# Kernel optimization log

Measured on AMD Instinct MI355X. Metric: run time of the kernel, lower is better.

The kernel has to match this reference:

```python
import jax, jax.numpy as jnp
import numpy as np
import math

B, S, E = 4, 2048, 1024


def setup_inputs() -> dict:
    key = jax.random.key(0)
    ks = jax.random.split(key, 9)
    x = jax.random.normal(ks[0], (B, S, E), dtype=jnp.float32)
    # causal boolean mask, broadcast over batch: True = keep
    mask = jnp.broadcast_to(jnp.tril(jnp.ones((S, S), dtype=bool)), (B, S, S))
    sc = 1.0 / math.sqrt(E)
    Wq = jax.random.normal(ks[1], (E, E), dtype=jnp.float32) * sc
    bq = jnp.zeros((E,), dtype=jnp.float32)
    Wk = jax.random.normal(ks[2], (E, E), dtype=jnp.float32) * sc
    bk = jnp.zeros((E,), dtype=jnp.float32)
    Wv = jax.random.normal(ks[3], (E, E), dtype=jnp.float32) * sc
    bv = jnp.zeros((E,), dtype=jnp.float32)
    gamma = jnp.ones((E,), dtype=jnp.float32)
    beta = jnp.zeros((E,), dtype=jnp.float32)
    return {"x": x, "mask": mask, "Wq": Wq, "bq": bq, "Wk": Wk, "bk": bk,
            "Wv": Wv, "bv": bv, "gamma": gamma, "beta": beta}


def reference(x, mask, Wq, bq, Wk, bk, Wv, bv, gamma, beta):
    E_ = x.shape[-1]
    q = jnp.einsum('bse,fe->bsf', x, Wq) + bq
    k = jnp.einsum('bse,fe->bsf', x, Wk) + bk
    v = jnp.einsum('bse,fe->bsf', x, Wv) + bv
    scores = jnp.einsum('bqe,bke->bqk', q, k) / jnp.sqrt(jnp.float32(E_))
    scores = jnp.where(mask, scores, -jnp.inf)
    probs = jax.nn.softmax(scores, axis=-1)
    attn = jnp.einsum('bqk,bke->bqe', probs, v)
    y = attn + x
    # LayerNorm over last dim, eps matches torch default 1e-5
    mu = jnp.mean(y, axis=-1, keepdims=True)
    var = jnp.mean(jnp.square(y - mu), axis=-1, keepdims=True)
    return (y - mu) / jnp.sqrt(var + 1e-5) * gamma + beta
```

## Files before the change

kernel.cpp:

```cpp
#include <hip/hip_runtime.h>
#include <hip/hip_bf16.h>
#include <stdint.h>

#define B_ 4
#define S_ 2048
#define E_ 1024
#define BS_ (B_*S_)

using bf16x8 = __attribute__((ext_vector_type(8))) __bf16;
using f32x4  = __attribute__((ext_vector_type(4))) float;

__constant__ int pv_mt[24] = {7,8,9,10,11,12,13,14,15,15,14,6,13,5,12,4,11,3,10,2,9,1,8,0};
__constant__ int pv_ck[24] = {0,0,0,0,0,0,0,0,0, 1, 1,0, 1,0, 1,0, 1,0, 1,0, 1,0, 1,0};

__device__ __forceinline__ unsigned short f2bf(float f) {
  unsigned int u = __float_as_uint(f);
  u += 0x7fffu + ((u >> 16) & 1u);
  return (unsigned short)(u >> 16);
}
__device__ __forceinline__ float bf2f(unsigned short h) {
  return __uint_as_float(((unsigned int)h) << 16);
}

__device__ __forceinline__ void gld16(const unsigned short* g, unsigned short* l) {
  __builtin_amdgcn_global_load_lds((__attribute__((address_space(1))) void*)(void*)g,
                                   (__attribute__((address_space(3))) void*)l, 16, 0, 0);
}

__global__ __launch_bounds__(256) void prep_all(
    const float* __restrict__ x,
    const float* __restrict__ Wq, const float* __restrict__ Wk, const float* __restrict__ Wv,
    const float* __restrict__ bq, const float* __restrict__ bk, const float* __restrict__ bv,
    unsigned short* __restrict__ xb, unsigned short* __restrict__ Wb, float* __restrict__ bb,
    float* __restrict__ lz) {
  const int i = blockIdx.x * 256 + threadIdx.x;
  const int nx4 = BS_ * E_ / 4, nw4 = E_ * E_ / 4;
  if (i < nx4) {
    const float4 v = ((const float4*)x)[i];
    ushort4 o;
    o.x = f2bf(v.x); o.y = f2bf(v.y); o.z = f2bf(v.z); o.w = f2bf(v.w);
    ((ushort4*)xb)[i] = o;
  } else if (i < nx4 + 3 * nw4) {
    const int j = i - nx4;
    const int m = j / nw4, jj = j - m * nw4;
    const float* src = (m == 0) ? Wq : (m == 1) ? Wk : Wv;
    const float4 v = ((const float4*)src)[jj];
    ushort4 o;
    o.x = f2bf(v.x); o.y = f2bf(v.y); o.z = f2bf(v.z); o.w = f2bf(v.w);
    ((ushort4*)Wb)[j] = o;
  } else {
    const int j = i - nx4 - 3 * nw4;
    if (j < 3 * E_) bb[j] = (j < E_) ? bq[j] : (j < 2 * E_) ? bk[j - E_] : bv[j - 2 * E_];
    else { const int k = j - 3 * E_; if (k < BS_) lz[k] = 0.f; }
  }
}

template<int EPI>
__device__ __forceinline__ void gemm_body(
    const unsigned short* __restrict__ A, const unsigned short* __restrict__ Bm,
    float* __restrict__ Cf,
    unsigned short* __restrict__ Cb, unsigned short* __restrict__ VtOut,
    const float* __restrict__ bias,
    int K, int lda, int ldb, int ldc,
    long sA, long sB, long sC, float scale)
{
  constexpr int BM = 128, BN = 128, BK = 64;
  __shared__ __align__(16) unsigned short As[BM * BK];
  __shared__ __align__(16) unsigned short Bs[BN * BK];

  int mt, nt, ck = 0, bz;
  if (EPI == 1) {
    const int sig = (blockIdx.x & 7) * 68 + (blockIdx.x >> 3);
    bz = sig / 136;
    const int rem = sig - bz * 136;
    const int M = (rem >= 78) ? 3 : (rem >= 36) ? 2 : (rem >= 10) ? 1 : 0;
    const int cumM = (M == 3) ? 78 : (M == 2) ? 36 : (M == 1) ? 10 : 0;
    const int inner = rem - cumM;
    if (inner < 16 * M) {
      const int N = inner >> 4, t2 = inner & 15;
      mt = 4 * M + (t2 >> 2); nt = 4 * N + (t2 & 3);
    } else {
      const int t2 = inner - 16 * M;
      const int ml = (t2 >= 6) ? 3 : (t2 >= 3) ? 2 : (t2 >= 1) ? 1 : 0;
      const int nl = t2 - (ml * (ml + 1)) / 2;
      mt = 4 * M + ml; nt = 4 * M + nl;
    }
  } else if (EPI == 2) {
    mt = pv_mt[blockIdx.y]; ck = pv_ck[blockIdx.y]; nt = blockIdx.x; bz = blockIdx.z;
  } else {
    mt = blockIdx.y; nt = blockIdx.x; bz = blockIdx.z;
  }
  A  += sA * bz;
  Bm += sB * bz;
  const int m0 = mt * BM, n0 = nt * BN;
  const int k0s  = (EPI == 2 && ck) ? 1024 : 0;
  const int kend = (EPI == 2) ? (ck ? m0 + BM : min(1024, m0 + BM)) : K;

  const int t = threadIdx.x;
  const int lane = t & 63, wave = t >> 6;
  const int wr = wave >> 1, wc = wave & 1;
  const int q = lane >> 4, r = lane & 15;

  const int srow   = lane >> 3;
  const int schunk = (lane & 7) ^ srow;
  const long ga0 = (long)(m0 + wave * 32 + srow) * lda + schunk * 8;
  const long gb0 = (long)(n0 + wave * 32 + srow) * ldb + schunk * 8;

  f32x4 acc[4][4] = {};

  for (int k0 = k0s; k0 < kend; k0 += BK) {
#pragma unroll
    for (int s = 0; s < 4; ++s) {
      gld16(A  + ga0 + (long)s * 8 * lda + k0, &As[(wave * 32 + s * 8) * 64]);
      gld16(Bm + gb0 + (long)s * 8 * ldb + k0, &Bs[(wave * 32 + s * 8) * 64]);
    }
    __syncthreads();
#pragma unroll
    for (int kk = 0; kk < BK; kk += 32) {
      bf16x8 af[4], bfr[4];
      const int cq = (kk >> 3) + q;
#pragma unroll
      for (int i = 0; i < 4; ++i) {
        const int row = wr * 64 + i * 16 + r;
        af[i] = *(const bf16x8*)&As[(row * 8 + (cq ^ (r & 7))) * 8];
      }
#pragma unroll
      for (int j = 0; j < 4; ++j) {
        const int row = wc * 64 + j * 16 + r;
        bfr[j] = *(const bf16x8*)&Bs[(row * 8 + (cq ^ (r & 7))) * 8];
      }
#pragma unroll
      for (int i = 0; i < 4; ++i)
#pragma unroll
        for (int j = 0; j < 4; ++j)
          acc[i][j] = __builtin_amdgcn_mfma_f32_16x16x32_bf16(af[i], bfr[j], acc[i][j], 0, 0, 0);
    }
    __syncthreads();
  }

  if (EPI == 0) {
    if (n0 < 2 * E_) {
#pragma unroll
    for (int i = 0; i < 4; ++i)
#pragma unroll
      for (int j = 0; j < 4; ++j) {
        const int col = n0 + wc * 64 + j * 16 + r;
        const float bia = bias[col];
#pragma unroll
        for (int e = 0; e < 4; ++e) {
          const int rowg = m0 + wr * 64 + i * 16 + q * 4 + e;
          Cb[(long)rowg * ldc + col] = f2bf(acc[i][j][e] + bia);
        }
      }
    } else {
      unsigned short* scr = As + wave * 2048;
      const int bb = m0 >> 11;
      const int sbase = (m0 & (S_ - 1)) + wr * 64;
#pragma unroll
      for (int j = 0; j < 4; ++j) {
        const int e_base = n0 - 2 * E_ + wc * 64 + j * 16;
        const float bj = bias[n0 + wc * 64 + j * 16 + r];
#pragma unroll
        for (int i = 0; i < 4; ++i) {
          const int c = 2 * i + (q >> 1);
          const int slot = c ^ (r & 7);
          ushort4 o;
          o.x = f2bf(acc[i][j][0] + bj);
          o.y = f2bf(acc[i][j][1] + bj);
          o.z = f2bf(acc[i][j][2] + bj);
          o.w = f2bf(acc[i][j][3] + bj);
          *(ushort4*)&scr[r * 72 + slot * 8 + (q & 1) * 4] = o;
        }
#pragma unroll
        for (int it = 0; it < 2; ++it) {
          const int er = it * 8 + (lane >> 3);
          const int w = lane & 7;
          const bf16x8 vv = *(const bf16x8*)&scr[er * 72 + w * 8];
          const int so = (w ^ (er & 7)) * 8;
          *(bf16x8*)&VtOut[((long)bb * E_ + e_base + er) * S_ + sbase + so] = vv;
        }
      }
    }
  } else if (EPI == 1) {
    Cb += sC * bz;
    float* lv = Cf + (long)bz * S_;
#pragma unroll
    for (int i = 0; i < 4; ++i) {
      float rs[4] = {0.f, 0.f, 0.f, 0.f};
#pragma unroll
      for (int j = 0; j < 4; ++j) {
        const int col = n0 + wc * 64 + j * 16 + r;
#pragma unroll
        for (int e = 0; e < 4; ++e) {
          const int rowg = m0 + wr * 64 + i * 16 + q * 4 + e;
          float p = 0.f;
          if (col <= rowg) p = __expf(fminf(acc[i][j][e] * scale, 60.f));
          Cb[(long)rowg * ldc + col] = f2bf(p);
          rs[e] += p;
        }
      }
#pragma unroll
      for (int e = 0; e < 4; ++e) {
        float s = rs[e];
        s += __shfl_xor(s, 1); s += __shfl_xor(s, 2);
        s += __shfl_xor(s, 4); s += __shfl_xor(s, 8);
        if (r == 0) atomicAdd(&lv[m0 + wr * 64 + i * 16 + q * 4 + e], s);
      }
    }
  } else {
    const float* lv = Cf + (long)bz * S_;
    unsigned short* dst = (ck ? VtOut : Cb) + sC * bz;
#pragma unroll
    for (int i = 0; i < 4; ++i) {
      const int rb = m0 + wr * 64 + i * 16 + q * 4;
      const float4 l4 = *(const float4*)&lv[rb];
      const float r0 = 1.f / l4.x, r1 = 1.f / l4.y, r2 = 1.f / l4.z, r3 = 1.f / l4.w;
#pragma unroll
      for (int j = 0; j < 4; ++j) {
        const int col = n0 + wc * 64 + j * 16 + r;
        dst[(long)(rb + 0) * ldc + col] = f2bf(acc[i][j][0] * r0);
        dst[(long)(rb + 1) * ldc + col] = f2bf(acc[i][j][1] * r1);
        dst[(long)(rb + 2) * ldc + col] = f2bf(acc[i][j][2] * r2);
        dst[(long)(rb + 3) * ldc + col] = f2bf(acc[i][j][3] * r3);
      }
    }
  }
}

__global__ __launch_bounds__(256, 4) void gemm_qkv(
    const unsigned short* A, const unsigned short* Bm, float* Cf,
    unsigned short* Cb, unsigned short* VtOut, const float* bias,
    int K, int lda, int ldb, int ldc, long sA, long sB, long sC, float scale) {
  gemm_body<0>(A, Bm, Cf, Cb, VtOut, bias, K, lda, ldb, ldc, sA, sB, sC, scale);
}
__global__ __launch_bounds__(256, 4) void gemm_sc(
    const unsigned short* A, const unsigned short* Bm, float* Cf,
    unsigned short* Cb, unsigned short* VtOut, const float* bias,
    int K, int lda, int ldb, int ldc, long sA, long sB, long sC, float scale) {
  gemm_body<1>(A, Bm, Cf, Cb, VtOut, bias, K, lda, ldb, ldc, sA, sB, sC, scale);
}
__global__ __launch_bounds__(256, 4) void gemm_pv(
    const unsigned short* A, const unsigned short* Bm, float* Cf,
    unsigned short* Cb, unsigned short* VtOut, const float* bias,
    int K, int lda, int ldb, int ldc, long sA, long sB, long sC, float scale) {
  gemm_body<2>(A, Bm, Cf, Cb, VtOut, bias, K, lda, ldb, ldc, sA, sB, sC, scale);
}

__global__ __launch_bounds__(256) void residual_ln(
    const unsigned short* __restrict__ attn, const unsigned short* __restrict__ attn2,
    const unsigned short* __restrict__ xb,
    const float* __restrict__ gamma, const float* __restrict__ beta,
    float* __restrict__ out) {
  __shared__ float rs[4], rs2[4];
  const long row = blockIdx.x;
  const int t = threadIdx.x;
  const int lane = t & 63, wave = t >> 6;
  const ushort4 a  = ((const ushort4*)(attn + row * E_))[t];
  const ushort4 xv = ((const ushort4*)(xb + row * E_))[t];
  ushort4 b2 = make_ushort4(0, 0, 0, 0);
  if ((row & (S_ - 1)) >= 1024) b2 = ((const ushort4*)(attn2 + row * E_))[t];
  const float y0 = bf2f(a.x) + bf2f(b2.x) + bf2f(xv.x);
  const float y1 = bf2f(a.y) + bf2f(b2.y) + bf2f(xv.y);
  const float y2 = bf2f(a.z) + bf2f(b2.z) + bf2f(xv.z);
  const float y3 = bf2f(a.w) + bf2f(b2.w) + bf2f(xv.w);
  float s  = y0 + y1 + y2 + y3;
  float s2 = y0 * y0 + y1 * y1 + y2 * y2 + y3 * y3;
#pragma unroll
  for (int o = 32; o; o >>= 1) { s += __shfl_xor(s, o); s2 += __shfl_xor(s2, o); }
  if (lane == 0) { rs[wave] = s; rs2[wave] = s2; }
  __syncthreads();
  s  = rs[0] + rs[1] + rs[2] + rs[3];
  s2 = rs2[0] + rs2[1] + rs2[2] + rs2[3];
  const float mu  = s * (1.0f / E_);
  const float var = s2 * (1.0f / E_) - mu * mu;
  const float inv = rsqrtf(var + 1e-5f);
  const float4 g  = ((const float4*)gamma)[t];
  const float4 be = ((const float4*)beta)[t];
  float4 o;
  o.x = (y0 - mu) * inv * g.x + be.x;
  o.y = (y1 - mu) * inv * g.y + be.y;
  o.z = (y2 - mu) * inv * g.z + be.z;
  o.w = (y3 - mu) * inv * g.w + be.w;
  ((float4*)(out + row * E_))[t] = o;
}

extern "C" void kernel_launch(void* const* d_in, const int* in_sizes, int n_in,
                              void* d_out, int out_size, void* d_ws, size_t ws_size,
                              hipStream_t stream) {
  const float* x  = (const float*)d_in[0];
  const float* Wq = (const float*)d_in[2];
  const float* bq = (const float*)d_in[3];
  const float* Wk = (const float*)d_in[4];
  const float* bk = (const float*)d_in[5];
  const float* Wv = (const float*)d_in[6];
  const float* bv = (const float*)d_in[7];
  const float* gamma = (const float*)d_in[8];
  const float* beta  = (const float*)d_in[9];
  float* out = (float*)d_out;

  char* ws = (char*)d_ws;
  size_t off = 0;
  auto alloc = [&](size_t bytes) { char* p = ws + off; off += (bytes + 255) & ~(size_t)255; return p; };
  unsigned short* xb    = (unsigned short*)alloc((size_t)BS_ * E_ * 2);
  unsigned short* Wqkvb = (unsigned short*)alloc((size_t)3 * E_ * E_ * 2);
  float*          bqkv  = (float*)alloc((size_t)3 * E_ * 4);
  unsigned short* Cqkv  = (unsigned short*)alloc((size_t)BS_ * 2 * E_ * 2);
  unsigned short* Vt    = (unsigned short*)alloc((size_t)BS_ * E_ * 2);
  unsigned short* Sc    = (unsigned short*)alloc((size_t)B_ * S_ * S_ * 2);
  float*          lrow  = (float*)alloc((size_t)BS_ * 4);
  unsigned short* attn  = (unsigned short*)Cqkv;
  unsigned short* attn2 = (unsigned short*)Cqkv + (size_t)BS_ * E_;

  const int nprep = BS_ * E_ / 4 + 3 * E_ * E_ / 4 + 3 * E_ + BS_;
  prep_all<<<dim3((nprep + 255) / 256), 256, 0, stream>>>(x, Wq, Wk, Wv, bq, bk, bv,
                                                          xb, Wqkvb, bqkv, lrow);

  dim3 g1(3 * E_ / 128, BS_ / 128, 1);
  gemm_qkv<<<g1, 256, 0, stream>>>(xb, Wqkvb, nullptr, Cqkv, Vt, bqkv,
                                   E_, E_, E_, 2 * E_, 0, 0, 0, 1.f);

  gemm_sc<<<dim3(544), 256, 0, stream>>>(Cqkv, Cqkv + E_, lrow, Sc, nullptr, nullptr,
                                         E_, 2 * E_, 2 * E_, S_,
                                         (long)S_ * 2 * E_, (long)S_ * 2 * E_, (long)S_ * S_,
                                         0.03125f);

  dim3 g3(E_ / 128, 24, B_);
  gemm_pv<<<g3, 256, 0, stream>>>(Sc, Vt, lrow, attn, attn2, nullptr,
                                  S_, S_, S_, E_,
                                  (long)S_ * S_, (long)S_ * E_, (long)S_ * E_, 1.f);

  residual_ln<<<dim3(BS_), 256, 0, stream>>>(attn, attn2, xb, gamma, beta, out);
}
```

Measured before the change: 268.5 us.

## Use 256x256 tiles with 8 waves and a 4-stage LDS pipeline

Rewrites the shared GEMM body to use 256x256 output tiles with 512 threads. K-slices of 32 are cycled through a 4-deep LDS ring buffer, with prefetch three tiles ahead and waits on vmcnt counts in place of the load/sync/compute loop. The causal-tile schedules for scores and PV are recomputed for the larger tiles. The V-transpose epilogue now writes directly instead of going through an LDS scratch. Larger tiles cut global traffic per FLOP but produce fewer blocks (144 for scores), and they waste more compute on masked diagonal tiles.

Result: slower. 335.0 us (+24.8%).

```diff
diff --git a/kernel.cpp b/kernel.cpp
--- a/kernel.cpp
+++ b/kernel.cpp
@@ -10,8 +10,8 @@
 using bf16x8 = __attribute__((ext_vector_type(8))) __bf16;
 using f32x4  = __attribute__((ext_vector_type(4))) float;
 
-__constant__ int pv_mt[24] = {7,8,9,10,11,12,13,14,15,15,14,6,13,5,12,4,11,3,10,2,9,1,8,0};
-__constant__ int pv_ck[24] = {0,0,0,0,0,0,0,0,0, 1, 1,0, 1,0, 1,0, 1,0, 1,0, 1,0, 1,0};
+__constant__ int pv_mt2[12] = {3,4,5,6,7,7,2,6,1,5,0,4};
+__constant__ int pv_ck2[12] = {0,0,0,0,0,1,0,1,0,1,0,1};
 
 __device__ __forceinline__ unsigned short f2bf(float f) {
   unsigned int u = __float_as_uint(f);
@@ -64,29 +64,19 @@
     int K, int lda, int ldb, int ldc,
     long sA, long sB, long sC, float scale)
 {
-  constexpr int BM = 128, BN = 128, BK = 64;
-  __shared__ __align__(16) unsigned short As[BM * BK];
-  __shared__ __align__(16) unsigned short Bs[BN * BK];
+  constexpr int BM = 256, BN = 256, BK = 32;
+  __shared__ __align__(16) unsigned short As[4][BM * BK];
+  __shared__ __align__(16) unsigned short Bs[4][BN * BK];
 
   int mt, nt, ck = 0, bz;
   if (EPI == 1) {
-    const int sig = (blockIdx.x & 7) * 68 + (blockIdx.x >> 3);
-    bz = sig / 136;
-    const int rem = sig - bz * 136;
-    const int M = (rem >= 78) ? 3 : (rem >= 36) ? 2 : (rem >= 10) ? 1 : 0;
-    const int cumM = (M == 3) ? 78 : (M == 2) ? 36 : (M == 1) ? 10 : 0;
-    const int inner = rem - cumM;
-    if (inner < 16 * M) {
-      const int N = inner >> 4, t2 = inner & 15;
-      mt = 4 * M + (t2 >> 2); nt = 4 * N + (t2 & 3);
-    } else {
-      const int t2 = inner - 16 * M;
-      const int ml = (t2 >= 6) ? 3 : (t2 >= 3) ? 2 : (t2 >= 1) ? 1 : 0;
-      const int nl = t2 - (ml * (ml + 1)) / 2;
-      mt = 4 * M + ml; nt = 4 * M + nl;
-    }
+    bz = blockIdx.x / 36;
+    int rem = blockIdx.x - bz * 36;
+    int m = 0, base2 = 0;
+    while (base2 + m + 1 <= rem) { base2 += m + 1; ++m; }
+    mt = m; nt = rem - base2;
   } else if (EPI == 2) {
-    mt = pv_mt[blockIdx.y]; ck = pv_ck[blockIdx.y]; nt = blockIdx.x; bz = blockIdx.z;
+    mt = pv_mt2[blockIdx.y]; ck = pv_ck2[blockIdx.y]; nt = blockIdx.x; bz = blockIdx.z;
   } else {
     mt = blockIdx.y; nt = blockIdx.x; bz = blockIdx.z;
   }
@@ -95,107 +85,109 @@
   const int m0 = mt * BM, n0 = nt * BN;
   const int k0s  = (EPI == 2 && ck) ? 1024 : 0;
   const int kend = (EPI == 2) ? (ck ? m0 + BM : min(1024, m0 + BM)) : K;
+  const int nT = (kend - k0s) >> 5;
 
   const int t = threadIdx.x;
   const int lane = t & 63, wave = t >> 6;
-  const int wr = wave >> 1, wc = wave & 1;
+  const int wr = wave >> 2, wc = wave & 3;
   const int q = lane >> 4, r = lane & 15;
 
-  const int srow   = lane >> 3;
-  const int schunk = (lane & 7) ^ srow;
-  const long ga0 = (long)(m0 + wave * 32 + srow) * lda + schunk * 8;
-  const long gb0 = (long)(n0 + wave * 32 + srow) * ldb + schunk * 8;
-
-  f32x4 acc[4][4] = {};
-
-  for (int k0 = k0s; k0 < kend; k0 += BK) {
-#pragma unroll
-    for (int s = 0; s < 4; ++s) {
-      gld16(A  + ga0 + (long)s * 8 * lda + k0, &As[(wave * 32 + s * 8) * 64]);
-      gld16(Bm + gb0 + (long)s * 8 * ldb + k0, &Bs[(wave * 32 + s * 8) * 64]);
-    }
-    __syncthreads();
-#pragma unroll
-    for (int kk = 0; kk < BK; kk += 32) {
-      bf16x8 af[4], bfr[4];
-      const int cq = (kk >> 3) + q;
-#pragma unroll
-      for (int i = 0; i < 4; ++i) {
-        const int row = wr * 64 + i * 16 + r;
-        af[i] = *(const bf16x8*)&As[(row * 8 + (cq ^ (r & 7))) * 8];
-      }
-#pragma unroll
-      for (int j = 0; j < 4; ++j) {
-        const int row = wc * 64 + j * 16 + r;
-        bfr[j] = *(const bf16x8*)&Bs[(row * 8 + (cq ^ (r & 7))) * 8];
-      }
-#pragma unroll
-      for (int i = 0; i < 4; ++i)
-#pragma unroll
-        for (int j = 0; j < 4; ++j)
-          acc[i][j] = __builtin_amdgcn_mfma_f32_16x16x32_bf16(af[i], bfr[j], acc[i][j], 0, 0, 0);
-    }
-    __syncthreads();
+  const int srow   = lane >> 2;
+  const int schunk = (lane & 3) ^ ((lane >> 3) & 3);
+  const long ga0 = (long)(m0 + wave * 32 + srow) * lda + schunk * 8 + k0s;
+  const long gb0 = (long)(n0 + wave * 32 + srow) * ldb + schunk * 8 + k0s;
+
+  auto STAGE = [&](int tile) {
+    const int buf = tile & 3;
+    const long ko = (long)tile << 5;
+    gld16(A  + ga0 + ko,            &As[buf][wave * 1024]);
+    gld16(A  + ga0 + 16 * lda + ko, &As[buf][wave * 1024 + 512]);
+    gld16(Bm + gb0 + ko,            &Bs[buf][wave * 1024]);
+    gld16(Bm + gb0 + 16 * ldb + ko, &Bs[buf][wave * 1024 + 512]);
+  };
+
+  f32x4 acc[8][4] = {};
+
+  STAGE(0); STAGE(1); STAGE(2);
+
+  const int ca    = (q ^ ((r >> 1) & 3)) * 8;
+  const int arow0 = wr * 128 + r;
+  const int brow0 = wc * 64 + r;
+
+  for (int tt = 0; tt < nT; ++tt) {
+    if (nT - tt > 2)       asm volatile("s_waitcnt vmcnt(8)" ::: "memory");
+    else if (nT - tt == 2) asm volatile("s_waitcnt vmcnt(4)" ::: "memory");
+    else                   asm volatile("s_waitcnt vmcnt(0)" ::: "memory");
+    __builtin_amdgcn_s_barrier();
+    asm volatile("" ::: "memory");
+    if (tt + 3 < nT) STAGE(tt + 3);
+
+    const unsigned short* as_ = As[tt & 3];
+    const unsigned short* bs_ = Bs[tt & 3];
+    bf16x8 af[8], bfv[4];
+#pragma unroll
+    for (int i = 0; i < 8; ++i)
+      af[i] = *(const bf16x8*)&as_[(arow0 + i * 16) * 32 + ca];
+#pragma unroll
+    for (int j = 0; j < 4; ++j)
+      bfv[j] = *(const bf16x8*)&bs_[(brow0 + j * 16) * 32 + ca];
+
+    __builtin_amdgcn_s_setprio(1);
+#pragma unroll
+    for (int i = 0; i < 8; ++i)
+#pragma unroll
+      for (int j = 0; j < 4; ++j)
+        acc[i][j] = __builtin_amdgcn_mfma_f32_16x16x32_bf16(af[i], bfv[j], acc[i][j], 0, 0, 0);
+    __builtin_amdgcn_s_setprio(0);
   }
 
   if (EPI == 0) {
     if (n0 < 2 * E_) {
 #pragma unroll
-    for (int i = 0; i < 4; ++i)
+      for (int i = 0; i < 8; ++i)
+#pragma unroll
+        for (int j = 0; j < 4; ++j) {
+          const int col = n0 + wc * 64 + j * 16 + r;
+          const float bia = bias[col];
+          const int rowg = m0 + wr * 128 + i * 16 + q * 4;
+#pragma unroll
+          for (int e = 0; e < 4; ++e)
+            Cb[(long)(rowg + e) * ldc + col] = f2bf(acc[i][j][e] + bia);
+        }
+    } else {
+      const int bb = m0 >> 11;
+      const int sb = (m0 & (S_ - 1)) + wr * 128;
 #pragma unroll
       for (int j = 0; j < 4; ++j) {
         const int col = n0 + wc * 64 + j * 16 + r;
         const float bia = bias[col];
-#pragma unroll
-        for (int e = 0; e < 4; ++e) {
-          const int rowg = m0 + wr * 64 + i * 16 + q * 4 + e;
-          Cb[(long)rowg * ldc + col] = f2bf(acc[i][j][e] + bia);
-        }
-      }
-    } else {
-      unsigned short* scr = As + wave * 2048;
-      const int bb = m0 >> 11;
-      const int sbase = (m0 & (S_ - 1)) + wr * 64;
-#pragma unroll
-      for (int j = 0; j < 4; ++j) {
-        const int e_base = n0 - 2 * E_ + wc * 64 + j * 16;
-        const float bj = bias[n0 + wc * 64 + j * 16 + r];
-#pragma unroll
-        for (int i = 0; i < 4; ++i) {
-          const int c = 2 * i + (q >> 1);
-          const int slot = c ^ (r & 7);
+        const long ebase = (long)bb * E_ + (col - 2 * E_);
+#pragma unroll
+        for (int i = 0; i < 8; ++i) {
           ushort4 o;
-          o.x = f2bf(acc[i][j][0] + bj);
-          o.y = f2bf(acc[i][j][1] + bj);
-          o.z = f2bf(acc[i][j][2] + bj);
-          o.w = f2bf(acc[i][j][3] + bj);
-          *(ushort4*)&scr[r * 72 + slot * 8 + (q & 1) * 4] = o;
-        }
-#pragma unroll
-        for (int it = 0; it < 2; ++it) {
-          const int er = it * 8 + (lane >> 3);
-          const int w = lane & 7;
-          const bf16x8 vv = *(const bf16x8*)&scr[er * 72 + w * 8];
-          const int so = (w ^ (er & 7)) * 8;
-          *(bf16x8*)&VtOut[((long)bb * E_ + e_base + er) * S_ + sbase + so] = vv;
+          o.x = f2bf(acc[i][j][0] + bia);
+          o.y = f2bf(acc[i][j][1] + bia);
+          o.z = f2bf(acc[i][j][2] + bia);
+          o.w = f2bf(acc[i][j][3] + bia);
+          *(ushort4*)&VtOut[ebase * S_ + sb + i * 16 + q * 4] = o;
         }
       }
     }
   } else if (EPI == 1) {
-    Cb += sC * bz;
+    unsigned short* Cbz = Cb + sC * bz;
     float* lv = Cf + (long)bz * S_;
 #pragma unroll
-    for (int i = 0; i < 4; ++i) {
+    for (int i = 0; i < 8; ++i) {
       float rs[4] = {0.f, 0.f, 0.f, 0.f};
+      const int rowg0 = m0 + wr * 128 + i * 16 + q * 4;
 #pragma unroll
       for (int j = 0; j < 4; ++j) {
         const int col = n0 + wc * 64 + j * 16 + r;
 #pragma unroll
         for (int e = 0; e < 4; ++e) {
-          const int rowg = m0 + wr * 64 + i * 16 + q * 4 + e;
           float p = 0.f;
-          if (col <= rowg) p = __expf(fminf(acc[i][j][e] * scale, 60.f));
-          Cb[(long)rowg * ldc + col] = f2bf(p);
+          if (col <= rowg0 + e) p = __expf(fminf(acc[i][j][e] * scale, 60.f));
+          Cbz[(long)(rowg0 + e) * ldc + col] = f2bf(p);
           rs[e] += p;
         }
       }
@@ -204,15 +196,15 @@
         float s = rs[e];
         s += __shfl_xor(s, 1); s += __shfl_xor(s, 2);
         s += __shfl_xor(s, 4); s += __shfl_xor(s, 8);
-        if (r == 0) atomicAdd(&lv[m0 + wr * 64 + i * 16 + q * 4 + e], s);
+        if (r == 0) atomicAdd(&lv[rowg0 + e], s);
       }
     }
   } else {
     const float* lv = Cf + (long)bz * S_;
     unsigned short* dst = (ck ? VtOut : Cb) + sC * bz;
 #pragma unroll
-    for (int i = 0; i < 4; ++i) {
-      const int rb = m0 + wr * 64 + i * 16 + q * 4;
+    for (int i = 0; i < 8; ++i) {
+      const int rb = m0 + wr * 128 + i * 16 + q * 4;
       const float4 l4 = *(const float4*)&lv[rb];
       const float r0 = 1.f / l4.x, r1 = 1.f / l4.y, r2 = 1.f / l4.z, r3 = 1.f / l4.w;
 #pragma unroll
@@ -227,19 +219,19 @@
   }
 }
 
-__global__ __launch_bounds__(256, 4) void gemm_qkv(
+__global__ __launch_bounds__(512, 2) void gemm_qkv(
     const unsigned short* A, const unsigned short* Bm, float* Cf,
     unsigned short* Cb, unsigned short* VtOut, const float* bias,
     int K, int lda, int ldb, int ldc, long sA, long sB, long sC, float scale) {
   gemm_body<0>(A, Bm, Cf, Cb, VtOut, bias, K, lda, ldb, ldc, sA, sB, sC, scale);
 }
-__global__ __launch_bounds__(256, 4) void gemm_sc(
+__global__ __launch_bounds__(512, 2) void gemm_sc(
     const unsigned short* A, const unsigned short* Bm, float* Cf,
     unsigned short* Cb, unsigned short* VtOut, const float* bias,
     int K, int lda, int ldb, int ldc, long sA, long sB, long sC, float scale) {
   gemm_body<1>(A, Bm, Cf, Cb, VtOut, bias, K, lda, ldb, ldc, sA, sB, sC, scale);
 }
-__global__ __launch_bounds__(256, 4) void gemm_pv(
+__global__ __launch_bounds__(512, 2) void gemm_pv(
     const unsigned short* A, const unsigned short* Bm, float* Cf,
     unsigned short* Cb, unsigned short* VtOut, const float* bias,
     int K, int lda, int ldb, int ldc, long sA, long sB, long sC, float scale) {
@@ -315,17 +307,17 @@
   prep_all<<<dim3((nprep + 255) / 256), 256, 0, stream>>>(x, Wq, Wk, Wv, bq, bk, bv,
                                                           xb, Wqkvb, bqkv, lrow);
 
-  dim3 g1(3 * E_ / 128, BS_ / 128, 1);
-  gemm_qkv<<<g1, 256, 0, stream>>>(xb, Wqkvb, nullptr, Cqkv, Vt, bqkv,
+  dim3 g1(3 * E_ / 256, BS_ / 256, 1);
+  gemm_qkv<<<g1, 512, 0, stream>>>(xb, Wqkvb, nullptr, Cqkv, Vt, bqkv,
                                    E_, E_, E_, 2 * E_, 0, 0, 0, 1.f);
 
-  gemm_sc<<<dim3(544), 256, 0, stream>>>(Cqkv, Cqkv + E_, lrow, Sc, nullptr, nullptr,
+  gemm_sc<<<dim3(144), 512, 0, stream>>>(Cqkv, Cqkv + E_, lrow, Sc, nullptr, nullptr,
                                          E_, 2 * E_, 2 * E_, S_,
                                          (long)S_ * 2 * E_, (long)S_ * 2 * E_, (long)S_ * S_,
                                          0.03125f);
 
-  dim3 g3(E_ / 128, 24, B_);
-  gemm_pv<<<g3, 256, 0, stream>>>(Sc, Vt, lrow, attn, attn2, nullptr,
+  dim3 g3(E_ / 256, 12, B_);
+  gemm_pv<<<g3, 512, 0, stream>>>(Sc, Vt, lrow, attn, attn2, nullptr,
                                   S_, S_, S_, E_,
                                   (long)S_ * S_, (long)S_ * E_, (long)S_ * E_, 1.f);
 
```
